# Optimization experiments

Hardware: AMD Instinct MI355X
Metric: run time of the kernel (lower is better)

## Reference

```python
import jax, jax.numpy as jnp
import numpy as np

S_GRID = 14.0
L_COORD = 5.0
L_NOOBJ = 0.5
B = 2


def _xywh2xyxy(b):
    # b: [..., 4] with (x, y, w, h); x,y are divided by S per the original module
    xy = b[..., :2] / S_GRID
    wh = b[..., 2:4]
    return jnp.concatenate([xy - 0.5 * wh, xy + 0.5 * wh], axis=-1)


def setup_inputs() -> dict:
    key = jax.random.key(0)
    k1, k2, k3, k4 = jax.random.split(key, 4)
    N, S, C = 4096, 14, 20
    pred_tensor = jax.random.uniform(k1, (N, S, S, B * 5 + C), dtype=jnp.float32, minval=0.05, maxval=1.0)
    target_boxes = jax.random.uniform(k2, (N, S, S, 4), dtype=jnp.float32, minval=0.05, maxval=1.0)
    target_cls = jax.random.normal(k3, (N, S, S, C), dtype=jnp.float32)
    has_object_map = jax.random.randint(k4, (N, S, S), 0, 2).astype(jnp.bool_)
    return {"pred_tensor": pred_tensor, "target_boxes": target_boxes,
            "target_cls": target_cls, "has_object_map": has_object_map}


def reference(pred_tensor, target_boxes, target_cls, has_object_map):
    N = pred_tensor.shape[0]
    mask = has_object_map                      # [N,S,S] bool
    maskf = mask.astype(pred_tensor.dtype)
    pb = pred_tensor[..., :B * 5].reshape(*pred_tensor.shape[:3], B, 5)  # [N,S,S,B,5]
    pc = pred_tensor[..., B * 5:]              # [N,S,S,20]

    # class loss: masked sum of squared errors over classes
    cls_loss = jnp.sum(maskf * jnp.sum((target_cls - pc) ** 2, axis=-1))

    # no-object loss: conf^2 on cells without objects, summed over both boxes
    conf = pb[..., 4]                          # [N,S,S,B]
    no_obj_loss = L_NOOBJ * jnp.sum(jnp.where(~mask[..., None], conf, 0.0) ** 2)

    # per-cell IoU of target vs each of the B predicted boxes (diag of original NxM)
    t_xyxy = _xywh2xyxy(target_boxes)          # [N,S,S,4]
    p_xyxy = _xywh2xyxy(pb[..., :4])           # [N,S,S,B,4]
    lt = jnp.maximum(t_xyxy[..., None, :2], p_xyxy[..., :2])
    rb = jnp.minimum(t_xyxy[..., None, 2:], p_xyxy[..., 2:])
    wh = jnp.clip(rb - lt, 0.0)
    inter = wh[..., 0] * wh[..., 1]            # [N,S,S,B]
    area_t = (t_xyxy[..., 2] - t_xyxy[..., 0]) * (t_xyxy[..., 3] - t_xyxy[..., 1])
    area_p = (p_xyxy[..., 2] - p_xyxy[..., 0]) * (p_xyxy[..., 3] - p_xyxy[..., 1])
    iou = inter / (area_t[..., None] + area_p - inter)  # [N,S,S,B]

    best_iou = jnp.max(iou, axis=-1)           # [N,S,S]
    best_idx = jnp.argmax(iou, axis=-1)        # [N,S,S]
    best_box = jnp.take_along_axis(pb, best_idx[..., None, None], axis=3)[..., 0, :]  # [N,S,S,5]

    xy_diff = jnp.where(mask[..., None], best_box[..., :2] - target_boxes[..., :2], 0.0)
    wh_p = jnp.where(mask[..., None], best_box[..., 2:4], 1.0)
    wh_t = jnp.where(mask[..., None], target_boxes[..., 2:4], 1.0)
    reg_loss = L_COORD * (jnp.sum(xy_diff ** 2)
                          + jnp.sum((jnp.sqrt(wh_p) - jnp.sqrt(wh_t)) ** 2))

    # containing-object confidence loss: mse(best_iou, best_box_conf) on object cells
    containing_obj_loss = jnp.sum(jnp.where(mask, best_iou - best_box[..., 4], 0.0) ** 2)

    total_loss = (cls_loss + no_obj_loss + reg_loss + containing_obj_loss) / N
    return (total_loss, reg_loss, containing_obj_loss, no_obj_loss, cls_loss)
```

## Files before the change

kernel.cpp:

```cpp
#include <hip/hip_runtime.h>
#include <math.h>


#define BLOCK 256
#define WPB 4

__global__ __launch_bounds__(BLOCK, 6) void k_yolo(
    const float*  __restrict__ pred,
    const float4* __restrict__ tbox4,
    const float4* __restrict__ tcls4,
    const int*    __restrict__ mask,
    float4*       __restrict__ partial,
    int n_cells)
{
    const int tid  = threadIdx.x;
    const int cell = blockIdx.x * BLOCK + tid;
    const bool valid = cell < n_cells;

    float cls = 0.f, noobj = 0.f, reg = 0.f, cont = 0.f;

    if (valid) {
        const float2* pc2 = reinterpret_cast<const float2*>(pred + (size_t)cell * 30);
        const float4* t4  = tcls4 + (size_t)cell * 5;

        const int    mflag = mask[cell];
        const float4 tb    = tbox4[cell];
        float2 v0  = pc2[0],  v1  = pc2[1],  v2  = pc2[2],  v3  = pc2[3],  v4  = pc2[4];
        float2 v5  = pc2[5],  v6  = pc2[6],  v7  = pc2[7],  v8  = pc2[8],  v9  = pc2[9];
        float2 v10 = pc2[10], v11 = pc2[11], v12 = pc2[12], v13 = pc2[13], v14 = pc2[14];
        float4 tc0 = t4[0], tc1 = t4[1], tc2 = t4[2], tc3 = t4[3], tc4 = t4[4];

        if (mflag) {
            float txc = tb.x / 14.0f, tyc = tb.y / 14.0f;
            float t0 = txc - 0.5f * tb.z, t1 = tyc - 0.5f * tb.w;
            float t2c = txc + 0.5f * tb.z, t3 = tyc + 0.5f * tb.w;
            float area_t = (t2c - t0) * (t3 - t1);
            float bx[2] = { v0.x, v2.y }, by[2] = { v0.y, v3.x };
            float bw[2] = { v1.x, v3.y }, bh[2] = { v1.y, v4.x };
            float bcf[2] = { v2.x, v4.y };
            float iou[2];
            #pragma unroll
            for (int b = 0; b < 2; ++b) {
                float px = bx[b] / 14.0f, py = by[b] / 14.0f;
                float q0 = px - 0.5f * bw[b], q1 = py - 0.5f * bh[b];
                float q2 = px + 0.5f * bw[b], q3 = py + 0.5f * bh[b];
                float lt0 = fmaxf(t0, q0), lt1 = fmaxf(t1, q1);
                float rb0 = fminf(t2c, q2), rb1 = fminf(t3, q3);
                float ww = fmaxf(rb0 - lt0, 0.f), hh = fmaxf(rb1 - lt1, 0.f);
                float inter = ww * hh;
                float area_p = (q2 - q0) * (q3 - q1);
                iou[b] = inter / (area_t + area_p - inter);
            }
            int bi = (iou[1] > iou[0]) ? 1 : 0;
            float dx = bx[bi] - tb.x, dy = by[bi] - tb.y;
            float swd = sqrtf(bw[bi]) - sqrtf(tb.z);
            float shd = sqrtf(bh[bi]) - sqrtf(tb.w);
            reg = 5.0f * (dx*dx + dy*dy + swd*swd + shd*shd);
            float dco = iou[bi] - bcf[bi];
            cont = dco * dco;

            float d;
            d = tc0.x - v5.x;  cls = fmaf(d, d, cls);
            d = tc0.y - v5.y;  cls = fmaf(d, d, cls);
            d = tc0.z - v6.x;  cls = fmaf(d, d, cls);
            d = tc0.w - v6.y;  cls = fmaf(d, d, cls);
            d = tc1.x - v7.x;  cls = fmaf(d, d, cls);
            d = tc1.y - v7.y;  cls = fmaf(d, d, cls);
            d = tc1.z - v8.x;  cls = fmaf(d, d, cls);
            d = tc1.w - v8.y;  cls = fmaf(d, d, cls);
            d = tc2.x - v9.x;  cls = fmaf(d, d, cls);
            d = tc2.y - v9.y;  cls = fmaf(d, d, cls);
            d = tc2.z - v10.x; cls = fmaf(d, d, cls);
            d = tc2.w - v10.y; cls = fmaf(d, d, cls);
            d = tc3.x - v11.x; cls = fmaf(d, d, cls);
            d = tc3.y - v11.y; cls = fmaf(d, d, cls);
            d = tc3.z - v12.x; cls = fmaf(d, d, cls);
            d = tc3.w - v12.y; cls = fmaf(d, d, cls);
            d = tc4.x - v13.x; cls = fmaf(d, d, cls);
            d = tc4.y - v13.y; cls = fmaf(d, d, cls);
            d = tc4.z - v14.x; cls = fmaf(d, d, cls);
            d = tc4.w - v14.y; cls = fmaf(d, d, cls);
        } else {
            noobj = 0.5f * (v2.x * v2.x + v4.y * v4.y);
        }
    }

    #pragma unroll
    for (int off = 32; off; off >>= 1) {
        cls   += __shfl_down(cls,   off, 64);
        noobj += __shfl_down(noobj, off, 64);
        reg   += __shfl_down(reg,   off, 64);
        cont  += __shfl_down(cont,  off, 64);
    }
    __shared__ float4 swr[WPB];
    const int lane = tid & 63, w = tid >> 6;
    if (lane == 0) swr[w] = make_float4(cls, noobj, reg, cont);
    __syncthreads();
    if (tid == 0) {
        float4 a = swr[0];
        #pragma unroll
        for (int i = 1; i < WPB; ++i) {
            float4 b = swr[i];
            a.x += b.x; a.y += b.y; a.z += b.z; a.w += b.w;
        }
        partial[blockIdx.x] = a;
    }
}

__global__ __launch_bounds__(BLOCK) void k_final(
    const float4* __restrict__ partial, int nblocks,
    float* __restrict__ out, float invN)
{
    float4 acc = make_float4(0.f, 0.f, 0.f, 0.f);
    for (int b = threadIdx.x; b < nblocks; b += BLOCK) {
        float4 v = partial[b];
        acc.x += v.x; acc.y += v.y; acc.z += v.z; acc.w += v.w;
    }
    #pragma unroll
    for (int off = 32; off; off >>= 1) {
        acc.x += __shfl_down(acc.x, off, 64);
        acc.y += __shfl_down(acc.y, off, 64);
        acc.z += __shfl_down(acc.z, off, 64);
        acc.w += __shfl_down(acc.w, off, 64);
    }
    __shared__ float4 sw[WPB];
    int lane = threadIdx.x & 63, w = threadIdx.x >> 6;
    if (lane == 0) sw[w] = acc;
    __syncthreads();
    if (threadIdx.x == 0) {
        float cls = 0.f, noobj = 0.f, reg = 0.f, cont = 0.f;
        #pragma unroll
        for (int i = 0; i < WPB; ++i) {
            cls += sw[i].x; noobj += sw[i].y; reg += sw[i].z; cont += sw[i].w;
        }
        out[0] = (cls + noobj + reg + cont) * invN;
        out[1] = reg;
        out[2] = cont;
        out[3] = noobj;
        out[4] = cls;
    }
}

extern "C" void kernel_launch(void* const* d_in, const int* in_sizes, int n_in,
                              void* d_out, int out_size, void* d_ws, size_t ws_size,
                              hipStream_t stream) {
    const float*  pred  = (const float*)d_in[0];
    const float4* tbox4 = (const float4*)d_in[1];
    const float4* tcls4 = (const float4*)d_in[2];
    const int*    mask  = (const int*)d_in[3];
    float* out = (float*)d_out;
    float4* partial = (float4*)d_ws;

    int n_cells = in_sizes[3];
    int N = in_sizes[0] / (14 * 14 * 30);
    int nblocks = (n_cells + BLOCK - 1) / BLOCK;

    hipLaunchKernelGGL(k_yolo, dim3(nblocks), dim3(BLOCK), 0, stream,
                       pred, tbox4, tcls4, mask, partial, n_cells);
    hipLaunchKernelGGL(k_final, dim3(1), dim3(BLOCK), 0, stream,
                       partial, nblocks, out, 1.0f / (float)N);
}
```

Measured before the change: 203.6 us.

## Process two cells per thread with float4 loads and lower occupancy bound

Each thread now handles a pair of adjacent cells, so the 30-float prediction and 20-float class rows for two cells can be read with full 16-byte float4 loads instead of float2 loads. The mask and box reads are widened to int2 and paired float4 loads, and a scheduling barrier keeps all loads issued before the compute. This halves the block count and raises per-thread register use (launch bounds relaxed from 6 to 2 waves), trading occupancy for wider, more aligned memory transactions in this bandwidth-bound reduction. An odd trailing cell is handled by a scalar fallback path.

```diff
diff --git a/kernel.cpp b/kernel.cpp
--- a/kernel.cpp
+++ b/kernel.cpp
@@ -3,85 +3,135 @@
 
 
 #define BLOCK 256
-#define WPB 4
-
-__global__ __launch_bounds__(BLOCK, 6) void k_yolo(
-    const float*  __restrict__ pred,
-    const float4* __restrict__ tbox4,
-    const float4* __restrict__ tcls4,
-    const int*    __restrict__ mask,
-    float4*       __restrict__ partial,
+
+#define CELL(PB, TB, tbv, mf) do {                                            \
+    if (mf) {                                                                 \
+        float txc = tbv.x / 14.0f, tyc = tbv.y / 14.0f;                       \
+        float t0_ = txc - 0.5f * tbv.z, t1_ = tyc - 0.5f * tbv.w;             \
+        float t2_ = txc + 0.5f * tbv.z, t3_ = tyc + 0.5f * tbv.w;             \
+        float area_t = (t2_ - t0_) * (t3_ - t1_);                             \
+        float iou[2];                                                         \
+        _Pragma("unroll")                                                     \
+        for (int b_ = 0; b_ < 2; ++b_) {                                      \
+            float px = pf[PB + 5*b_ + 0] / 14.0f;                             \
+            float py = pf[PB + 5*b_ + 1] / 14.0f;                             \
+            float w_ = pf[PB + 5*b_ + 2], h_ = pf[PB + 5*b_ + 3];             \
+            float q0_ = px - 0.5f * w_, q1_ = py - 0.5f * h_;                 \
+            float q2_ = px + 0.5f * w_, q3_ = py + 0.5f * h_;                 \
+            float lt0 = fmaxf(t0_, q0_), lt1 = fmaxf(t1_, q1_);               \
+            float rb0 = fminf(t2_, q2_), rb1 = fminf(t3_, q3_);               \
+            float ww = fmaxf(rb0 - lt0, 0.f), hh = fmaxf(rb1 - lt1, 0.f);     \
+            float inter = ww * hh;                                            \
+            float area_p = (q2_ - q0_) * (q3_ - q1_);                         \
+            iou[b_] = inter / (area_t + area_p - inter);                      \
+        }                                                                     \
+        int bi_ = (iou[1] > iou[0]) ? 1 : 0;          \
+        float bx_ = bi_ ? pf[PB+5] : pf[PB+0];                                \
+        float by_ = bi_ ? pf[PB+6] : pf[PB+1];                                \
+        float bw_ = bi_ ? pf[PB+7] : pf[PB+2];                                \
+        float bh_ = bi_ ? pf[PB+8] : pf[PB+3];                                \
+        float bc_ = bi_ ? pf[PB+9] : pf[PB+4];                                \
+        float biou = bi_ ? iou[1] : iou[0];                                   \
+        float dx_ = bx_ - tbv.x, dy_ = by_ - tbv.y;                           \
+        float swd = sqrtf(bw_) - sqrtf(tbv.z);                                \
+        float shd = sqrtf(bh_) - sqrtf(tbv.w);                                \
+        reg = fmaf(5.0f, dx_*dx_ + dy_*dy_ + swd*swd + shd*shd, reg);         \
+        float dco = biou - bc_;                                               \
+        cont = fmaf(dco, dco, cont);                                          \
+        _Pragma("unroll")                                                     \
+        for (int k_ = 0; k_ < 20; ++k_) {                                     \
+            float d_ = tf[TB + k_] - pf[PB + 10 + k_];                        \
+            cls = fmaf(d_, d_, cls);                                          \
+        }                                                                     \
+    } else {                                                                  \
+        noobj += 0.5f * (pf[PB+4]*pf[PB+4] + pf[PB+9]*pf[PB+9]);              \
+    }                                                                         \
+} while (0)
+
+__global__ __launch_bounds__(BLOCK, 2) void k_yolo(
+    const float* __restrict__ pred,
+    const float* __restrict__ tbox,
+    const float* __restrict__ tcls,
+    const int*   __restrict__ mask,
+    float4*      __restrict__ partial,
     int n_cells)
 {
-    const int tid  = threadIdx.x;
-    const int cell = blockIdx.x * BLOCK + tid;
-    const bool valid = cell < n_cells;
+    const int tid = threadIdx.x;
+    const long long p = (long long)blockIdx.x * BLOCK + tid;
 
     float cls = 0.f, noobj = 0.f, reg = 0.f, cont = 0.f;
 
-    if (valid) {
-        const float2* pc2 = reinterpret_cast<const float2*>(pred + (size_t)cell * 30);
-        const float4* t4  = tcls4 + (size_t)cell * 5;
-
-        const int    mflag = mask[cell];
-        const float4 tb    = tbox4[cell];
-        float2 v0  = pc2[0],  v1  = pc2[1],  v2  = pc2[2],  v3  = pc2[3],  v4  = pc2[4];
-        float2 v5  = pc2[5],  v6  = pc2[6],  v7  = pc2[7],  v8  = pc2[8],  v9  = pc2[9];
-        float2 v10 = pc2[10], v11 = pc2[11], v12 = pc2[12], v13 = pc2[13], v14 = pc2[14];
-        float4 tc0 = t4[0], tc1 = t4[1], tc2 = t4[2], tc3 = t4[3], tc4 = t4[4];
-
-        if (mflag) {
-            float txc = tb.x / 14.0f, tyc = tb.y / 14.0f;
-            float t0 = txc - 0.5f * tb.z, t1 = tyc - 0.5f * tb.w;
-            float t2c = txc + 0.5f * tb.z, t3 = tyc + 0.5f * tb.w;
-            float area_t = (t2c - t0) * (t3 - t1);
-            float bx[2] = { v0.x, v2.y }, by[2] = { v0.y, v3.x };
-            float bw[2] = { v1.x, v3.y }, bh[2] = { v1.y, v4.x };
-            float bcf[2] = { v2.x, v4.y };
+    if (2 * p + 1 < (long long)n_cells) {
+        const float4* pq = reinterpret_cast<const float4*>(pred) + p * 15;
+        const float4* tq = reinterpret_cast<const float4*>(tcls) + p * 10;
+        const float4* bq = reinterpret_cast<const float4*>(tbox) + p * 2;
+
+        int2   mm = reinterpret_cast<const int2*>(mask)[p];
+        float4 b0 = bq[0], b1 = bq[1];
+        float4 q0  = pq[0],  q1  = pq[1],  q2  = pq[2],  q3  = pq[3];
+        float4 q4  = pq[4],  q5  = pq[5],  q6  = pq[6],  q7  = pq[7];
+        float4 q8  = pq[8],  q9  = pq[9],  q10 = pq[10], q11 = pq[11];
+        float4 q12 = pq[12], q13 = pq[13], q14 = pq[14];
+        float4 t0 = tq[0], t1 = tq[1], t2 = tq[2], t3 = tq[3], t4 = tq[4];
+        float4 t5 = tq[5], t6 = tq[6], t7 = tq[7], t8 = tq[8], t9 = tq[9];
+        __builtin_amdgcn_sched_barrier(0);
+
+        const float pf[60] = {
+            q0.x,q0.y,q0.z,q0.w,   q1.x,q1.y,q1.z,q1.w,   q2.x,q2.y,q2.z,q2.w,
+            q3.x,q3.y,q3.z,q3.w,   q4.x,q4.y,q4.z,q4.w,   q5.x,q5.y,q5.z,q5.w,
+            q6.x,q6.y,q6.z,q6.w,   q7.x,q7.y,q7.z,q7.w,   q8.x,q8.y,q8.z,q8.w,
+            q9.x,q9.y,q9.z,q9.w,   q10.x,q10.y,q10.z,q10.w, q11.x,q11.y,q11.z,q11.w,
+            q12.x,q12.y,q12.z,q12.w, q13.x,q13.y,q13.z,q13.w, q14.x,q14.y,q14.z,q14.w };
+        const float tf[40] = {
+            t0.x,t0.y,t0.z,t0.w, t1.x,t1.y,t1.z,t1.w, t2.x,t2.y,t2.z,t2.w,
+            t3.x,t3.y,t3.z,t3.w, t4.x,t4.y,t4.z,t4.w, t5.x,t5.y,t5.z,t5.w,
+            t6.x,t6.y,t6.z,t6.w, t7.x,t7.y,t7.z,t7.w, t8.x,t8.y,t8.z,t8.w,
+            t9.x,t9.y,t9.z,t9.w };
+
+        CELL(0,  0,  b0, mm.x);
+        CELL(30, 20, b1, mm.y);
+    } else if (2 * p < (long long)n_cells) {
+        const long long c = 2 * p;
+        const float* f = pred + c * 30;
+        const int mf = mask[c];
+        const float4 tbv = reinterpret_cast<const float4*>(tbox)[c];
+        if (mf) {
+            float txc = tbv.x / 14.0f, tyc = tbv.y / 14.0f;
+            float t0_ = txc - 0.5f * tbv.z, t1_ = tyc - 0.5f * tbv.w;
+            float t2_ = txc + 0.5f * tbv.z, t3_ = tyc + 0.5f * tbv.w;
+            float area_t = (t2_ - t0_) * (t3_ - t1_);
             float iou[2];
             #pragma unroll
-            for (int b = 0; b < 2; ++b) {
-                float px = bx[b] / 14.0f, py = by[b] / 14.0f;
-                float q0 = px - 0.5f * bw[b], q1 = py - 0.5f * bh[b];
-                float q2 = px + 0.5f * bw[b], q3 = py + 0.5f * bh[b];
-                float lt0 = fmaxf(t0, q0), lt1 = fmaxf(t1, q1);
-                float rb0 = fminf(t2c, q2), rb1 = fminf(t3, q3);
+            for (int b_ = 0; b_ < 2; ++b_) {
+                float px = f[5*b_+0] / 14.0f, py = f[5*b_+1] / 14.0f;
+                float w_ = f[5*b_+2], h_ = f[5*b_+3];
+                float q0_ = px - 0.5f * w_, q1_ = py - 0.5f * h_;
+                float q2_ = px + 0.5f * w_, q3_ = py + 0.5f * h_;
+                float lt0 = fmaxf(t0_, q0_), lt1 = fmaxf(t1_, q1_);
+                float rb0 = fminf(t2_, q2_), rb1 = fminf(t3_, q3_);
                 float ww = fmaxf(rb0 - lt0, 0.f), hh = fmaxf(rb1 - lt1, 0.f);
                 float inter = ww * hh;
-                float area_p = (q2 - q0) * (q3 - q1);
-                iou[b] = inter / (area_t + area_p - inter);
+                float area_p = (q2_ - q0_) * (q3_ - q1_);
+                iou[b_] = inter / (area_t + area_p - inter);
             }
-            int bi = (iou[1] > iou[0]) ? 1 : 0;
-            float dx = bx[bi] - tb.x, dy = by[bi] - tb.y;
-            float swd = sqrtf(bw[bi]) - sqrtf(tb.z);
-            float shd = sqrtf(bh[bi]) - sqrtf(tb.w);
-            reg = 5.0f * (dx*dx + dy*dy + swd*swd + shd*shd);
-            float dco = iou[bi] - bcf[bi];
-            cont = dco * dco;
-
-            float d;
-            d = tc0.x - v5.x;  cls = fmaf(d, d, cls);
-            d = tc0.y - v5.y;  cls = fmaf(d, d, cls);
-            d = tc0.z - v6.x;  cls = fmaf(d, d, cls);
-            d = tc0.w - v6.y;  cls = fmaf(d, d, cls);
-            d = tc1.x - v7.x;  cls = fmaf(d, d, cls);
-            d = tc1.y - v7.y;  cls = fmaf(d, d, cls);
-            d = tc1.z - v8.x;  cls = fmaf(d, d, cls);
-            d = tc1.w - v8.y;  cls = fmaf(d, d, cls);
-            d = tc2.x - v9.x;  cls = fmaf(d, d, cls);
-            d = tc2.y - v9.y;  cls = fmaf(d, d, cls);
-            d = tc2.z - v10.x; cls = fmaf(d, d, cls);
-            d = tc2.w - v10.y; cls = fmaf(d, d, cls);
-            d = tc3.x - v11.x; cls = fmaf(d, d, cls);
-            d = tc3.y - v11.y; cls = fmaf(d, d, cls);
-            d = tc3.z - v12.x; cls = fmaf(d, d, cls);
-            d = tc3.w - v12.y; cls = fmaf(d, d, cls);
-            d = tc4.x - v13.x; cls = fmaf(d, d, cls);
-            d = tc4.y - v13.y; cls = fmaf(d, d, cls);
-            d = tc4.z - v14.x; cls = fmaf(d, d, cls);
-            d = tc4.w - v14.y; cls = fmaf(d, d, cls);
+            int bi_ = (iou[1] > iou[0]) ? 1 : 0;
+            float bx_ = f[5*bi_+0], by_ = f[5*bi_+1];
+            float bw_ = f[5*bi_+2], bh_ = f[5*bi_+3], bc_ = f[5*bi_+4];
+            float biou = bi_ ? iou[1] : iou[0];
+            float dx_ = bx_ - tbv.x, dy_ = by_ - tbv.y;
+            float swd = sqrtf(bw_) - sqrtf(tbv.z);
+            float shd = sqrtf(bh_) - sqrtf(tbv.w);
+            reg = fmaf(5.0f, dx_*dx_ + dy_*dy_ + swd*swd + shd*shd, reg);
+            float dco = biou - bc_;
+            cont = fmaf(dco, dco, cont);
+            const float* g = tcls + c * 20;
+            #pragma unroll
+            for (int k_ = 0; k_ < 20; ++k_) {
+                float d_ = g[k_] - f[10 + k_];
+                cls = fmaf(d_, d_, cls);
+            }
         } else {
-            noobj = 0.5f * (v2.x * v2.x + v4.y * v4.y);
+            noobj += 0.5f * (f[4]*f[4] + f[9]*f[9]);
         }
     }
 
@@ -92,14 +142,14 @@
         reg   += __shfl_down(reg,   off, 64);
         cont  += __shfl_down(cont,  off, 64);
     }
-    __shared__ float4 swr[WPB];
+    __shared__ float4 swr[4];
     const int lane = tid & 63, w = tid >> 6;
     if (lane == 0) swr[w] = make_float4(cls, noobj, reg, cont);
     __syncthreads();
     if (tid == 0) {
         float4 a = swr[0];
         #pragma unroll
-        for (int i = 1; i < WPB; ++i) {
+        for (int i = 1; i < 4; ++i) {
             float4 b = swr[i];
             a.x += b.x; a.y += b.y; a.z += b.z; a.w += b.w;
         }
@@ -107,12 +157,12 @@
     }
 }
 
-__global__ __launch_bounds__(BLOCK) void k_final(
+__global__ __launch_bounds__(256) void k_final(
     const float4* __restrict__ partial, int nblocks,
     float* __restrict__ out, float invN)
 {
     float4 acc = make_float4(0.f, 0.f, 0.f, 0.f);
-    for (int b = threadIdx.x; b < nblocks; b += BLOCK) {
+    for (int b = threadIdx.x; b < nblocks; b += 256) {
         float4 v = partial[b];
         acc.x += v.x; acc.y += v.y; acc.z += v.z; acc.w += v.w;
     }
@@ -123,14 +173,14 @@
         acc.z += __shfl_down(acc.z, off, 64);
         acc.w += __shfl_down(acc.w, off, 64);
     }
-    __shared__ float4 sw[WPB];
+    __shared__ float4 sw[4];
     int lane = threadIdx.x & 63, w = threadIdx.x >> 6;
     if (lane == 0) sw[w] = acc;
     __syncthreads();
     if (threadIdx.x == 0) {
         float cls = 0.f, noobj = 0.f, reg = 0.f, cont = 0.f;
         #pragma unroll
-        for (int i = 0; i < WPB; ++i) {
+        for (int i = 0; i < 4; ++i) {
             cls += sw[i].x; noobj += sw[i].y; reg += sw[i].z; cont += sw[i].w;
         }
         out[0] = (cls + noobj + reg + cont) * invN;
@@ -144,19 +194,20 @@
 extern "C" void kernel_launch(void* const* d_in, const int* in_sizes, int n_in,
                               void* d_out, int out_size, void* d_ws, size_t ws_size,
                               hipStream_t stream) {
-    const float*  pred  = (const float*)d_in[0];
-    const float4* tbox4 = (const float4*)d_in[1];
-    const float4* tcls4 = (const float4*)d_in[2];
-    const int*    mask  = (const int*)d_in[3];
+    const float* pred = (const float*)d_in[0];
+    const float* tbox = (const float*)d_in[1];
+    const float* tcls = (const float*)d_in[2];
+    const int*   mask = (const int*)d_in[3];
     float* out = (float*)d_out;
     float4* partial = (float4*)d_ws;
 
     int n_cells = in_sizes[3];
     int N = in_sizes[0] / (14 * 14 * 30);
-    int nblocks = (n_cells + BLOCK - 1) / BLOCK;
+    long long nslots = ((long long)n_cells + 1) / 2;
+    int nblocks = (int)((nslots + BLOCK - 1) / BLOCK);
 
     hipLaunchKernelGGL(k_yolo, dim3(nblocks), dim3(BLOCK), 0, stream,
-                       pred, tbox4, tcls4, mask, partial, n_cells);
-    hipLaunchKernelGGL(k_final, dim3(1), dim3(BLOCK), 0, stream,
+                       pred, tbox, tcls, mask, partial, n_cells);
+    hipLaunchKernelGGL(k_final, dim3(1), dim3(256), 0, stream,
                        partial, nblocks, out, 1.0f / (float)N);
 }
```

Result: no change. 206.2 us (+1.3%).
